# Performance work log

Hardware: AMD Instinct MI355X
Metric: run time of the kernel (lower is better)

## Reference

```python
import jax, jax.numpy as jnp
import numpy as np

B, L, S, D_MODEL, H = 2, 2048, 2048, 1024, 16
D_HEAD = D_MODEL // H  # 64


def setup_inputs() -> dict:
    key = jax.random.key(0)
    ks = jax.random.split(key, 11)
    s = 0.02
    return {
        "queries": jax.random.normal(ks[0], (B, L, D_MODEL), jnp.float32),
        "keys": jax.random.normal(ks[1], (B, S, D_MODEL), jnp.float32),
        "values": jax.random.normal(ks[2], (B, S, D_MODEL), jnp.float32),
        # Linear weights stored as [in, out] (torch W.T), biases [out]
        "Wq": jax.random.normal(ks[3], (D_MODEL, H * D_HEAD), jnp.float32) * s,
        "bq": jnp.zeros((H * D_HEAD,), jnp.float32),
        "Wk": jax.random.normal(ks[4], (D_MODEL, H * D_HEAD), jnp.float32) * s,
        "bk": jnp.zeros((H * D_HEAD,), jnp.float32),
        "Wv": jax.random.normal(ks[5], (D_MODEL, H * D_HEAD), jnp.float32) * s,
        "bv": jnp.zeros((H * D_HEAD,), jnp.float32),
        "Wo": jax.random.normal(ks[6], (H * D_HEAD, D_MODEL), jnp.float32) * s,
        "bo": jnp.zeros((D_MODEL,), jnp.float32),
    }


def reference(queries, keys, values, Wq, bq, Wk, bk, Wv, bv, Wo, bo):
    b, l, _ = queries.shape
    _, s, _ = keys.shape
    # QKV projections -> [B, L/S, H, D_HEAD]
    q = (queries @ Wq + bq).reshape(b, l, H, D_HEAD)
    k = (keys @ Wk + bk).reshape(b, s, H, D_HEAD)
    v = (values @ Wv + bv).reshape(b, s, H, D_HEAD)
    scale = 1.0 / jnp.sqrt(jnp.asarray(D_HEAD, q.dtype))
    # Full score matrix [B, H, L, S] (mask_flag=False -> no causal mask)
    scores = jnp.einsum("blhe,bshe->bhls", q, k)
    A = jax.nn.softmax(scale * scores, axis=-1)  # dropout is identity at eval
    out = jnp.einsum("bhls,bshd->blhd", A, v).reshape(b, l, H * D_HEAD)
    out = out @ Wo + bo
    return out, A
```

## Files before the change

### kernel.cpp

```cpp
#include <hip/hip_runtime.h>


typedef __attribute__((ext_vector_type(8))) __bf16 bf16x8;
typedef __attribute__((ext_vector_type(4))) float f32x4;

__device__ __forceinline__ unsigned int f2bf_u(float f) {
  unsigned int u = __float_as_uint(f);
  return (u + 0x7FFFu + ((u >> 16) & 1u)) >> 16;
}
__device__ __forceinline__ float bf2f(unsigned int h) {
  return __uint_as_float(h << 16);
}
__device__ __forceinline__ unsigned int pack2(float lo, float hi) {
  return (f2bf_u(hi) << 16) | f2bf_u(lo);
}
__device__ __forceinline__ f32x4 mfma16(bf16x8 a, bf16x8 b, f32x4 c) {
  return __builtin_amdgcn_mfma_f32_16x16x32_bf16(a, b, c, 0, 0, 0);
}
__device__ __forceinline__ void gll16(const void* g, void* l) {
  __builtin_amdgcn_global_load_lds(
      (const __attribute__((address_space(1))) unsigned int*)g,
      (__attribute__((address_space(3))) unsigned int*)l, 16, 0, 0);
}

__global__ __launch_bounds__(256) void transpose_w(
    const float* __restrict__ W0, const float* __restrict__ W1,
    const float* __restrict__ W2, const float* __restrict__ W3,
    unsigned short* __restrict__ T0, unsigned short* __restrict__ T1,
    unsigned short* __restrict__ T2, unsigned short* __restrict__ T3) {
  const float* W; unsigned short* T;
  switch (blockIdx.z) {
    case 0: W = W0; T = T0; break;
    case 1: W = W1; T = T1; break;
    case 2: W = W2; T = T2; break;
    default: W = W3; T = T3; break;
  }
  __shared__ float tile[32][33];
  const int tx = threadIdx.x, ty = threadIdx.y;
  const int i0 = blockIdx.x * 32, o0 = blockIdx.y * 32;
  #pragma unroll
  for (int r = 0; r < 4; ++r)
    tile[ty + 8 * r][tx] = W[(size_t)(i0 + ty + 8 * r) * 1024 + o0 + tx];
  __syncthreads();
  #pragma unroll
  for (int r = 0; r < 4; ++r)
    T[(size_t)(o0 + ty + 8 * r) * 1024 + i0 + tx] =
        (unsigned short)f2bf_u(tile[tx][ty + 8 * r]);
}

struct GemmJob {
  const float* A;
  const unsigned short* BT;
  const float* bias;
  void* C;
  int omode;
};
struct GemmJobs { GemmJob j[3]; };

__global__ __launch_bounds__(256) void gemm_qkv(GemmJobs jobs, int M, int N, int K) {
  const GemmJob jb = jobs.j[blockIdx.z];
  __shared__ unsigned short As[128][40];
  __shared__ unsigned short Bs[128][32];
  const int tid = threadIdx.x;
  const int lane = tid & 63, wid = tid >> 6;
  const int l15 = lane & 15, l4 = lane >> 4;
  const int m0 = blockIdx.x * 128, n0 = blockIdx.y * 128;
  const int wr = wid >> 1, wc = wid & 1;

  f32x4 acc[4][4];
  #pragma unroll
  for (int i = 0; i < 4; ++i)
    #pragma unroll
    for (int j = 0; j < 4; ++j) acc[i][j] = (f32x4){0.f, 0.f, 0.f, 0.f};

  const int nk = K >> 5;
  for (int kt = 0; kt < nk; ++kt) {
    #pragma unroll
    for (int c = 0; c < 4; ++c) {
      const int chunk = c * 256 + tid;
      const int row = chunk >> 3, col4 = chunk & 7;
      const float4 f = *(const float4*)(jb.A +
                                        (size_t)(m0 + row) * K + kt * 32 + col4 * 4);
      ushort4 o;
      o.x = (unsigned short)f2bf_u(f.x);
      o.y = (unsigned short)f2bf_u(f.y);
      o.z = (unsigned short)f2bf_u(f.z);
      o.w = (unsigned short)f2bf_u(f.w);
      *(ushort4*)&As[row][col4 * 4] = o;
    }
    #pragma unroll
    for (int c = 0; c < 2; ++c) {
      const int off = wid * 2048 + c * 1024;
      const int loff = off + lane * 16;
      const int row = loff >> 6, colb = loff & 63;
      gll16(jb.BT + (size_t)(n0 + row) * K + kt * 32 + colb / 2,
            (char*)&Bs[0][0] + off);
    }
    __syncthreads();
    bf16x8 af[4], bfr[4];
    #pragma unroll
    for (int i = 0; i < 4; ++i)
      af[i] = *(const bf16x8*)&As[wr * 64 + i * 16 + l15][l4 * 8];
    #pragma unroll
    for (int j = 0; j < 4; ++j)
      bfr[j] = *(const bf16x8*)&Bs[wc * 64 + j * 16 + l15][l4 * 8];
    #pragma unroll
    for (int i = 0; i < 4; ++i)
      #pragma unroll
      for (int j = 0; j < 4; ++j)
        acc[i][j] = mfma16(af[i], bfr[j], acc[i][j]);
    __syncthreads();
  }

  #pragma unroll
  for (int j = 0; j < 4; ++j) {
    const int col = n0 + wc * 64 + j * 16 + l15;
    const float bv = jb.bias[col];
    #pragma unroll
    for (int i = 0; i < 4; ++i) {
      const int rowb = m0 + wr * 64 + i * 16 + l4 * 4;
      if (jb.omode == 2) {
        const int bq = rowb >> 11, sq = rowb & 2047;
        const int hq = col >> 6, dq = col & 63;
        ushort4 o;
        o.x = (unsigned short)f2bf_u(acc[i][j][0] + bv);
        o.y = (unsigned short)f2bf_u(acc[i][j][1] + bv);
        o.z = (unsigned short)f2bf_u(acc[i][j][2] + bv);
        o.w = (unsigned short)f2bf_u(acc[i][j][3] + bv);
        *(ushort4*)((unsigned short*)jb.C +
                    ((size_t)((bq * 16 + hq) * 64 + dq) << 11) + sq) = o;
      } else {
        #pragma unroll
        for (int q = 0; q < 4; ++q)
          ((unsigned short*)jb.C)[(size_t)(rowb + q) * N + col] =
              (unsigned short)f2bf_u(acc[i][j][q] + bv);
      }
    }
  }
}

__global__ __launch_bounds__(256) void gemm_out(
    const unsigned short* __restrict__ Ap, const unsigned short* __restrict__ BT,
    const float* __restrict__ bias, float* __restrict__ Cp,
    int M, int N, int K) {
  __shared__ unsigned short As[128][32];
  __shared__ unsigned short Bs[128][32];
  const int tid = threadIdx.x;
  const int lane = tid & 63, wid = tid >> 6;
  const int l15 = lane & 15, l4 = lane >> 4;
  const int m0 = blockIdx.x * 128, n0 = blockIdx.y * 128;
  const int wr = wid >> 1, wc = wid & 1;

  f32x4 acc[4][4];
  #pragma unroll
  for (int i = 0; i < 4; ++i)
    #pragma unroll
    for (int j = 0; j < 4; ++j) acc[i][j] = (f32x4){0.f, 0.f, 0.f, 0.f};

  const int nk = K >> 5;
  for (int kt = 0; kt < nk; ++kt) {
    const unsigned short* G = (wid < 2) ? (Ap + (size_t)m0 * K)
                                        : (BT + (size_t)n0 * K);
    char* L = (wid < 2) ? (char*)&As[0][0] : (char*)&Bs[0][0];
    const int half = wid & 1;
    #pragma unroll
    for (int c = 0; c < 4; ++c) {
      const int off = half * 4096 + c * 1024;
      const int loff = off + lane * 16;
      const int row = loff >> 6, colb = loff & 63;
      gll16(G + (size_t)row * K + kt * 32 + colb / 2, L + off);
    }
    __syncthreads();
    bf16x8 af[4], bfr[4];
    #pragma unroll
    for (int i = 0; i < 4; ++i)
      af[i] = *(const bf16x8*)&As[wr * 64 + i * 16 + l15][l4 * 8];
    #pragma unroll
    for (int j = 0; j < 4; ++j)
      bfr[j] = *(const bf16x8*)&Bs[wc * 64 + j * 16 + l15][l4 * 8];
    #pragma unroll
    for (int i = 0; i < 4; ++i)
      #pragma unroll
      for (int j = 0; j < 4; ++j)
        acc[i][j] = mfma16(af[i], bfr[j], acc[i][j]);
    __syncthreads();
  }

  #pragma unroll
  for (int j = 0; j < 4; ++j) {
    const int col = n0 + wc * 64 + j * 16 + l15;
    const float bv = bias[col];
    #pragma unroll
    for (int i = 0; i < 4; ++i) {
      const int rowb = m0 + wr * 64 + i * 16 + l4 * 4;
      #pragma unroll
      for (int q = 0; q < 4; ++q)
        Cp[(size_t)(rowb + q) * N + col] = acc[i][j][q] + bv;
    }
  }
}

__global__ __launch_bounds__(512) void attn_pv(
    const unsigned short* __restrict__ Q, const unsigned short* __restrict__ K,
    const unsigned short* __restrict__ VT, float2* __restrict__ Mst,
    unsigned short* __restrict__ OutPre) {
  __shared__ unsigned short Kt[128][64];
  __shared__ unsigned short Vt[64][128];

  const int tid = threadIdx.x;
  const int w = tid >> 6, lane = tid & 63;
  const int l15 = lane & 15, l4 = lane >> 4;
  const int wgid = blockIdx.x;
  const int xcd = wgid & 7, j = wgid >> 3;
  const int bh = xcd * 4 + (j >> 4);
  const int b = bh >> 4, h = bh & 15;
  const int m0 = (j & 15) * 128;

  const unsigned short* Qp =
      Q + ((size_t)(b * 2048 + m0 + w * 16 + l15) << 10) + h * 64 + l4 * 8;
  const bf16x8 qf0 = *(const bf16x8*)Qp;
  const bf16x8 qf1 = *(const bf16x8*)(Qp + 32);

  const unsigned short* Kb = K + ((size_t)b << 21) + h * 64;
  const unsigned short* Vbh = VT + ((size_t)bh << 17);

  const int krow = lane >> 3;
  const int kcolb = (lane & 7) ^ krow;
  const int vrow = lane >> 4;

  float m_run = -3.0e38f, l_run = 0.f;
  f32x4 pv[4];
  #pragma unroll
  for (int nt = 0; nt < 4; ++nt) pv[nt] = (f32x4){0.f, 0.f, 0.f, 0.f};

  for (int t = 0; t < 16; ++t) {
    #pragma unroll
    for (int c = 0; c < 2; ++c) {
      const int r = w * 16 + c * 8 + krow;
      gll16(Kb + ((size_t)(t * 128 + r) << 10) + kcolb * 8,
            &Kt[w * 16 + c * 8][0]);
    }
    #pragma unroll
    for (int c = 0; c < 2; ++c) {
      const int d = w * 8 + c * 4 + vrow;
      const int vc = (lane & 15) ^ (d & 7);
      gll16(Vbh + ((size_t)d << 11) + t * 128 + vc * 8,
            &Vt[w * 8 + c * 4][0]);
    }
    __syncthreads();

    unsigned int sc16[16];
    float tmax = -3.0e38f;
    #pragma unroll
    for (int sub = 0; sub < 8; ++sub) {
      const int row = sub * 16 + l15;
      const bf16x8 k0 = *(const bf16x8*)&Kt[row][(l4 ^ (l15 & 7)) * 8];
      const bf16x8 k1 = *(const bf16x8*)&Kt[row][((l4 + 4) ^ (l15 & 7)) * 8];
      f32x4 a = {0.f, 0.f, 0.f, 0.f};
      a = mfma16(k0, qf0, a);
      a = mfma16(k1, qf1, a);
      const unsigned int u0 = f2bf_u(a[0] * 0.125f);
      const unsigned int u1 = f2bf_u(a[1] * 0.125f);
      const unsigned int u2 = f2bf_u(a[2] * 0.125f);
      const unsigned int u3 = f2bf_u(a[3] * 0.125f);
      sc16[sub * 2 + 0] = (u1 << 16) | u0;
      sc16[sub * 2 + 1] = (u3 << 16) | u2;
      tmax = fmaxf(tmax, fmaxf(fmaxf(bf2f(u0), bf2f(u1)),
                               fmaxf(bf2f(u2), bf2f(u3))));
    }
    tmax = fmaxf(tmax, __shfl_xor(tmax, 16));
    tmax = fmaxf(tmax, __shfl_xor(tmax, 32));
    const float m_new = fmaxf(m_run, tmax);
    const float f = __expf(m_run - m_new);
    m_run = m_new;
    float fr[4];
    #pragma unroll
    for (int r = 0; r < 4; ++r) fr[r] = __shfl(f, l4 * 4 + r);
    #pragma unroll
    for (int nt = 0; nt < 4; ++nt) {
      pv[nt][0] *= fr[0]; pv[nt][1] *= fr[1];
      pv[nt][2] *= fr[2]; pv[nt][3] *= fr[3];
    }
    l_run *= f;

    union EF { unsigned int u4[4]; bf16x8 v; } ef[4];
    #pragma unroll
    for (int kc = 0; kc < 4; ++kc) {
      #pragma unroll
      for (int half = 0; half < 2; ++half) {
        const unsigned int p0 = sc16[(kc * 2 + half) * 2 + 0];
        const unsigned int p1 = sc16[(kc * 2 + half) * 2 + 1];
        const float e0 = __expf(bf2f(p0 & 0xffffu) - m_new);
        const float e1 = __expf(bf2f(p0 >> 16) - m_new);
        const float e2 = __expf(bf2f(p1 & 0xffffu) - m_new);
        const float e3 = __expf(bf2f(p1 >> 16) - m_new);
        l_run += e0 + e1 + e2 + e3;
        ef[kc].u4[half * 2 + 0] = pack2(e0, e1);
        ef[kc].u4[half * 2 + 1] = pack2(e2, e3);
      }
    }

    #pragma unroll
    for (int nt = 0; nt < 4; ++nt) {
      const int d = nt * 16 + l15;
      #pragma unroll
      for (int kc = 0; kc < 4; ++kc) {
        const int c16a = (kc * 4 + (l4 >> 1)) ^ (d & 7);
        const int c16b = (kc * 4 + 2 + (l4 >> 1)) ^ (d & 7);
        union { unsigned int u4[4]; bf16x8 v; } vf;
        const uint2 va = *(const uint2*)&Vt[d][c16a * 8 + (l4 & 1) * 4];
        const uint2 vb = *(const uint2*)&Vt[d][c16b * 8 + (l4 & 1) * 4];
        vf.u4[0] = va.x; vf.u4[1] = va.y; vf.u4[2] = vb.x; vf.u4[3] = vb.y;
        pv[nt] = mfma16(ef[kc].v, vf.v, pv[nt]);
      }
    }
    __syncthreads();
  }

  float lsum = l_run;
  lsum += __shfl_xor(lsum, 16);
  lsum += __shfl_xor(lsum, 32);
  const float linv = 1.0f / lsum;
  if (lane < 16)
    Mst[(size_t)bh * 2048 + m0 + w * 16 + lane] = make_float2(m_run, linv);
  #pragma unroll
  for (int r = 0; r < 4; ++r) {
    const float lq = __shfl(linv, l4 * 4 + r);
    const size_t rowoff =
        ((size_t)(b * 2048 + m0 + w * 16 + l4 * 4 + r) << 10) + h * 64;
    #pragma unroll
    for (int nt = 0; nt < 4; ++nt)
      OutPre[rowoff + nt * 16 + l15] =
          (unsigned short)f2bf_u(pv[nt][r] * lq);
  }
}

__global__ __launch_bounds__(512) void attn_awrite(
    const unsigned short* __restrict__ Q, const unsigned short* __restrict__ K,
    const float2* __restrict__ Mst, float* __restrict__ Aout) {
  __shared__ float atile[16][136];
  const int tid = threadIdx.x;
  const int w = tid >> 6, lane = tid & 63;
  const int l15 = lane & 15, l4 = lane >> 4;
  const int wgid = blockIdx.x;
  const int xcd = wgid & 7, j = wgid >> 3;
  const int bh = xcd * 4 + (j >> 7);
  const int b = bh >> 4, h = bh & 15;
  const int m0 = (j & 127) * 16;

  const unsigned short* Qp =
      Q + ((size_t)(b * 2048 + m0 + l15) << 10) + h * 64 + l4 * 8;
  const bf16x8 qf0 = *(const bf16x8*)Qp;
  const bf16x8 qf1 = *(const bf16x8*)(Qp + 32);
  const unsigned short* Kb = K + ((size_t)b << 21) + h * 64;

  const float2 ml = Mst[(size_t)bh * 2048 + m0 + l15];
  const float mreg = ml.x, lreg = ml.y;

  float* Awg = Aout + ((size_t)bh << 22) + ((size_t)m0 << 11);
  const int frow = tid >> 5;
  const int fcol = (tid & 31) * 4;

  const unsigned short* kp0 = Kb + ((size_t)(w * 16 + l15) << 10) + l4 * 8;
  bf16x8 ck0 = *(const bf16x8*)kp0;
  bf16x8 ck1 = *(const bf16x8*)(kp0 + 32);
  #pragma unroll
  for (int i = 0; i < 16; ++i) {
    bf16x8 nk0, nk1;
    if (i < 15) {
      const unsigned short* kp =
          Kb + ((size_t)((i + 1) * 128 + w * 16 + l15) << 10) + l4 * 8;
      nk0 = *(const bf16x8*)kp;
      nk1 = *(const bf16x8*)(kp + 32);
    }
    f32x4 a = {0.f, 0.f, 0.f, 0.f};
    a = mfma16(ck0, qf0, a);
    a = mfma16(ck1, qf1, a);
    ck0 = nk0;
    ck1 = nk1;
    f32x4 av;
    #pragma unroll
    for (int q = 0; q < 4; ++q) {
      const float sb = bf2f(f2bf_u(a[q] * 0.125f));
      av[q] = __expf(sb - mreg) * lreg;
    }
    *(f32x4*)&atile[l15][w * 16 + l4 * 4] = av;
    __syncthreads();
    const f32x4 v = *(const f32x4*)&atile[frow][fcol];
    __builtin_nontemporal_store(
        v, (f32x4*)(Awg + ((size_t)frow << 11) + i * 128 + fcol));
    __syncthreads();
  }
}

extern "C" void kernel_launch(void* const* d_in, const int* in_sizes, int n_in,
                              void* d_out, int out_size, void* d_ws,
                              size_t ws_size, hipStream_t stream) {
  (void)in_sizes; (void)n_in; (void)out_size; (void)ws_size;
  const float* queries = (const float*)d_in[0];
  const float* keys    = (const float*)d_in[1];
  const float* values  = (const float*)d_in[2];
  const float* Wq = (const float*)d_in[3];  const float* bq = (const float*)d_in[4];
  const float* Wk = (const float*)d_in[5];  const float* bk = (const float*)d_in[6];
  const float* Wv = (const float*)d_in[7];  const float* bv = (const float*)d_in[8];
  const float* Wo = (const float*)d_in[9];  const float* bo = (const float*)d_in[10];

  float* out  = (float*)d_out;
  float* Aout = out + (size_t)2 * 2048 * 1024;

  char* ws = (char*)d_ws;
  unsigned short* WqT = (unsigned short*)(ws + 0);
  unsigned short* WkT = (unsigned short*)(ws + 2097152);
  unsigned short* WvT = (unsigned short*)(ws + 4194304);
  unsigned short* WoT = (unsigned short*)(ws + 6291456);
  unsigned short* Qb  = (unsigned short*)(ws + 8388608);
  unsigned short* Kbf = (unsigned short*)(ws + 16777216);
  unsigned short* VTb = (unsigned short*)(ws + 25165824);
  unsigned short* Op  = (unsigned short*)(ws + 33554432);
  float2* Mst = (float2*)(ws + 41943040);

  transpose_w<<<dim3(32, 32, 4), dim3(32, 8), 0, stream>>>(
      Wq, Wk, Wv, Wo, WqT, WkT, WvT, WoT);

  GemmJobs qkv;
  qkv.j[0] = {queries, WqT, bq, Qb, 0};
  qkv.j[1] = {keys,    WkT, bk, Kbf, 0};
  qkv.j[2] = {values,  WvT, bv, VTb, 2};
  gemm_qkv<<<dim3(32, 8, 3), 256, 0, stream>>>(qkv, 4096, 1024, 1024);

  attn_pv<<<dim3(512), 512, 0, stream>>>(Qb, Kbf, VTb, Mst, Op);
  attn_awrite<<<dim3(4096), 512, 0, stream>>>(Qb, Kbf, Mst, Aout);

  gemm_out<<<dim3(32, 8), 256, 0, stream>>>(
      Op, WoT, bo, out, 4096, 1024, 1024);
}
```

Baseline: 296.0 us.

## Double per-wave query rows in attn_pv and halve gemm_out N-tile

```diff
diff --git a/kernel.cpp b/kernel.cpp
--- a/kernel.cpp
+++ b/kernel.cpp
@@ -144,42 +144,45 @@
     const float* __restrict__ bias, float* __restrict__ Cp,
     int M, int N, int K) {
   __shared__ unsigned short As[128][32];
-  __shared__ unsigned short Bs[128][32];
+  __shared__ unsigned short Bs[64][32];
   const int tid = threadIdx.x;
-  const int lane = tid & 63, wid = tid >> 6;
+  const int lane = tid & 63, w = tid >> 6;
   const int l15 = lane & 15, l4 = lane >> 4;
-  const int m0 = blockIdx.x * 128, n0 = blockIdx.y * 128;
-  const int wr = wid >> 1, wc = wid & 1;
-
-  f32x4 acc[4][4];
-  #pragma unroll
-  for (int i = 0; i < 4; ++i)
+  const int m0 = blockIdx.x * 128, n0 = blockIdx.y * 64;
+
+  f32x4 acc[2][4];
+  #pragma unroll
+  for (int i = 0; i < 2; ++i)
     #pragma unroll
     for (int j = 0; j < 4; ++j) acc[i][j] = (f32x4){0.f, 0.f, 0.f, 0.f};
 
   const int nk = K >> 5;
   for (int kt = 0; kt < nk; ++kt) {
-    const unsigned short* G = (wid < 2) ? (Ap + (size_t)m0 * K)
-                                        : (BT + (size_t)n0 * K);
-    char* L = (wid < 2) ? (char*)&As[0][0] : (char*)&Bs[0][0];
-    const int half = wid & 1;
-    #pragma unroll
-    for (int c = 0; c < 4; ++c) {
-      const int off = half * 4096 + c * 1024;
+    #pragma unroll
+    for (int c = 0; c < 2; ++c) {
+      const int off = (w * 2 + c) * 1024;
       const int loff = off + lane * 16;
       const int row = loff >> 6, colb = loff & 63;
-      gll16(G + (size_t)row * K + kt * 32 + colb / 2, L + off);
-    }
-    __syncthreads();
-    bf16x8 af[4], bfr[4];
-    #pragma unroll
-    for (int i = 0; i < 4; ++i)
-      af[i] = *(const bf16x8*)&As[wr * 64 + i * 16 + l15][l4 * 8];
+      gll16(Ap + (size_t)(m0 + row) * K + kt * 32 + colb / 2,
+            (char*)&As[0][0] + off);
+    }
+    {
+      const int off = w * 1024;
+      const int loff = off + lane * 16;
+      const int row = loff >> 6, colb = loff & 63;
+      gll16(BT + (size_t)(n0 + row) * K + kt * 32 + colb / 2,
+            (char*)&Bs[0][0] + off);
+    }
+    __syncthreads();
+    bf16x8 af[2], bfr[4];
+    #pragma unroll
+    for (int i = 0; i < 2; ++i)
+      af[i] = *(const bf16x8*)&As[w * 32 + i * 16 + l15][l4 * 8];
     #pragma unroll
     for (int j = 0; j < 4; ++j)
-      bfr[j] = *(const bf16x8*)&Bs[wc * 64 + j * 16 + l15][l4 * 8];
-    #pragma unroll
-    for (int i = 0; i < 4; ++i)
+      bfr[j] = *(const bf16x8*)&Bs[j * 16 + l15][l4 * 8];
+    #pragma unroll
+    for (int i = 0; i < 2; ++i)
       #pragma unroll
       for (int j = 0; j < 4; ++j)
         acc[i][j] = mfma16(af[i], bfr[j], acc[i][j]);
@@ -188,11 +191,11 @@
 
   #pragma unroll
   for (int j = 0; j < 4; ++j) {
-    const int col = n0 + wc * 64 + j * 16 + l15;
+    const int col = n0 + j * 16 + l15;
     const float bv = bias[col];
     #pragma unroll
-    for (int i = 0; i < 4; ++i) {
-      const int rowb = m0 + wr * 64 + i * 16 + l4 * 4;
+    for (int i = 0; i < 2; ++i) {
+      const int rowb = m0 + w * 32 + i * 16 + l4 * 4;
       #pragma unroll
       for (int q = 0; q < 4; ++q)
         Cp[(size_t)(rowb + q) * N + col] = acc[i][j][q] + bv;
@@ -200,7 +203,7 @@
   }
 }
 
-__global__ __launch_bounds__(512) void attn_pv(
+__global__ __launch_bounds__(256) void attn_pv(
     const unsigned short* __restrict__ Q, const unsigned short* __restrict__ K,
     const unsigned short* __restrict__ VT, float2* __restrict__ Mst,
     unsigned short* __restrict__ OutPre) {
@@ -215,11 +218,16 @@
   const int bh = xcd * 4 + (j >> 4);
   const int b = bh >> 4, h = bh & 15;
   const int m0 = (j & 15) * 128;
-
-  const unsigned short* Qp =
-      Q + ((size_t)(b * 2048 + m0 + w * 16 + l15) << 10) + h * 64 + l4 * 8;
-  const bf16x8 qf0 = *(const bf16x8*)Qp;
-  const bf16x8 qf1 = *(const bf16x8*)(Qp + 32);
+  const int base = w * 32;
+
+  bf16x8 qf0[2], qf1[2];
+  #pragma unroll
+  for (int f = 0; f < 2; ++f) {
+    const unsigned short* Qp =
+        Q + ((size_t)(b * 2048 + m0 + base + f * 16 + l15) << 10) + h * 64 + l4 * 8;
+    qf0[f] = *(const bf16x8*)Qp;
+    qf1[f] = *(const bf16x8*)(Qp + 32);
+  }
 
   const unsigned short* Kb = K + ((size_t)b << 21) + h * 64;
   const unsigned short* Vbh = VT + ((size_t)bh << 17);
@@ -228,77 +236,88 @@
   const int kcolb = (lane & 7) ^ krow;
   const int vrow = lane >> 4;
 
-  float m_run = -3.0e38f, l_run = 0.f;
-  f32x4 pv[4];
-  #pragma unroll
-  for (int nt = 0; nt < 4; ++nt) pv[nt] = (f32x4){0.f, 0.f, 0.f, 0.f};
+  float m_run[2] = {-3.0e38f, -3.0e38f};
+  float l_run[2] = {0.f, 0.f};
+  f32x4 pv[2][4];
+  #pragma unroll
+  for (int f = 0; f < 2; ++f)
+    #pragma unroll
+    for (int nt = 0; nt < 4; ++nt) pv[f][nt] = (f32x4){0.f, 0.f, 0.f, 0.f};
 
   for (int t = 0; t < 16; ++t) {
     #pragma unroll
-    for (int c = 0; c < 2; ++c) {
-      const int r = w * 16 + c * 8 + krow;
+    for (int c = 0; c < 4; ++c) {
+      const int r = base + c * 8 + krow;
       gll16(Kb + ((size_t)(t * 128 + r) << 10) + kcolb * 8,
-            &Kt[w * 16 + c * 8][0]);
-    }
-    #pragma unroll
-    for (int c = 0; c < 2; ++c) {
-      const int d = w * 8 + c * 4 + vrow;
+            &Kt[base + c * 8][0]);
+    }
+    #pragma unroll
+    for (int c = 0; c < 4; ++c) {
+      const int d = w * 16 + c * 4 + vrow;
       const int vc = (lane & 15) ^ (d & 7);
       gll16(Vbh + ((size_t)d << 11) + t * 128 + vc * 8,
-            &Vt[w * 8 + c * 4][0]);
-    }
-    __syncthreads();
-
-    unsigned int sc16[16];
-    float tmax = -3.0e38f;
+            &Vt[w * 16 + c * 4][0]);
+    }
+    __syncthreads();
+
+    unsigned int sc16[2][16];
+    float tmax[2] = {-3.0e38f, -3.0e38f};
     #pragma unroll
     for (int sub = 0; sub < 8; ++sub) {
       const int row = sub * 16 + l15;
       const bf16x8 k0 = *(const bf16x8*)&Kt[row][(l4 ^ (l15 & 7)) * 8];
       const bf16x8 k1 = *(const bf16x8*)&Kt[row][((l4 + 4) ^ (l15 & 7)) * 8];
-      f32x4 a = {0.f, 0.f, 0.f, 0.f};
-      a = mfma16(k0, qf0, a);
-      a = mfma16(k1, qf1, a);
-      const unsigned int u0 = f2bf_u(a[0] * 0.125f);
-      const unsigned int u1 = f2bf_u(a[1] * 0.125f);
-      const unsigned int u2 = f2bf_u(a[2] * 0.125f);
-      const unsigned int u3 = f2bf_u(a[3] * 0.125f);
-      sc16[sub * 2 + 0] = (u1 << 16) | u0;
-      sc16[sub * 2 + 1] = (u3 << 16) | u2;
-      tmax = fmaxf(tmax, fmaxf(fmaxf(bf2f(u0), bf2f(u1)),
-                               fmaxf(bf2f(u2), bf2f(u3))));
-    }
-    tmax = fmaxf(tmax, __shfl_xor(tmax, 16));
-    tmax = fmaxf(tmax, __shfl_xor(tmax, 32));
-    const float m_new = fmaxf(m_run, tmax);
-    const float f = __expf(m_run - m_new);
-    m_run = m_new;
-    float fr[4];
-    #pragma unroll
-    for (int r = 0; r < 4; ++r) fr[r] = __shfl(f, l4 * 4 + r);
-    #pragma unroll
-    for (int nt = 0; nt < 4; ++nt) {
-      pv[nt][0] *= fr[0]; pv[nt][1] *= fr[1];
-      pv[nt][2] *= fr[2]; pv[nt][3] *= fr[3];
-    }
-    l_run *= f;
-
-    union EF { unsigned int u4[4]; bf16x8 v; } ef[4];
-    #pragma unroll
-    for (int kc = 0; kc < 4; ++kc) {
-      #pragma unroll
-      for (int half = 0; half < 2; ++half) {
-        const unsigned int p0 = sc16[(kc * 2 + half) * 2 + 0];
-        const unsigned int p1 = sc16[(kc * 2 + half) * 2 + 1];
-        const float e0 = __expf(bf2f(p0 & 0xffffu) - m_new);
-        const float e1 = __expf(bf2f(p0 >> 16) - m_new);
-        const float e2 = __expf(bf2f(p1 & 0xffffu) - m_new);
-        const float e3 = __expf(bf2f(p1 >> 16) - m_new);
-        l_run += e0 + e1 + e2 + e3;
-        ef[kc].u4[half * 2 + 0] = pack2(e0, e1);
-        ef[kc].u4[half * 2 + 1] = pack2(e2, e3);
+      #pragma unroll
+      for (int f = 0; f < 2; ++f) {
+        f32x4 a = {0.f, 0.f, 0.f, 0.f};
+        a = mfma16(k0, qf0[f], a);
+        a = mfma16(k1, qf1[f], a);
+        const unsigned int u0 = f2bf_u(a[0] * 0.125f);
+        const unsigned int u1 = f2bf_u(a[1] * 0.125f);
+        const unsigned int u2 = f2bf_u(a[2] * 0.125f);
+        const unsigned int u3 = f2bf_u(a[3] * 0.125f);
+        sc16[f][sub * 2 + 0] = (u1 << 16) | u0;
+        sc16[f][sub * 2 + 1] = (u3 << 16) | u2;
+        tmax[f] = fmaxf(tmax[f], fmaxf(fmaxf(bf2f(u0), bf2f(u1)),
+                                       fmaxf(bf2f(u2), bf2f(u3))));
       }
     }
+    #pragma unroll
+    for (int f = 0; f < 2; ++f) {
+      float tm = tmax[f];
+      tm = fmaxf(tm, __shfl_xor(tm, 16));
+      tm = fmaxf(tm, __shfl_xor(tm, 32));
+      const float m_new = fmaxf(m_run[f], tm);
+      const float fs = __expf(m_run[f] - m_new);
+      m_run[f] = m_new;
+      float fr[4];
+      #pragma unroll
+      for (int r = 0; r < 4; ++r) fr[r] = __shfl(fs, l4 * 4 + r);
+      #pragma unroll
+      for (int nt = 0; nt < 4; ++nt) {
+        pv[f][nt][0] *= fr[0]; pv[f][nt][1] *= fr[1];
+        pv[f][nt][2] *= fr[2]; pv[f][nt][3] *= fr[3];
+      }
+      l_run[f] *= fs;
+    }
+
+    union EF { unsigned int u4[4]; bf16x8 v; } ef[2][4];
+    #pragma unroll
+    for (int f = 0; f < 2; ++f)
+      #pragma unroll
+      for (int kc = 0; kc < 4; ++kc)
+        #pragma unroll
+        for (int half = 0; half < 2; ++half) {
+          const unsigned int p0 = sc16[f][(kc * 2 + half) * 2 + 0];
+          const unsigned int p1 = sc16[f][(kc * 2 + half) * 2 + 1];
+          const float e0 = __expf(bf2f(p0 & 0xffffu) - m_run[f]);
+          const float e1 = __expf(bf2f(p0 >> 16) - m_run[f]);
+          const float e2 = __expf(bf2f(p1 & 0xffffu) - m_run[f]);
+          const float e3 = __expf(bf2f(p1 >> 16) - m_run[f]);
+          l_run[f] += e0 + e1 + e2 + e3;
+          ef[f][kc].u4[half * 2 + 0] = pack2(e0, e1);
+          ef[f][kc].u4[half * 2 + 1] = pack2(e2, e3);
+        }
 
     #pragma unroll
     for (int nt = 0; nt < 4; ++nt) {
@@ -311,28 +330,38 @@
         const uint2 va = *(const uint2*)&Vt[d][c16a * 8 + (l4 & 1) * 4];
         const uint2 vb = *(const uint2*)&Vt[d][c16b * 8 + (l4 & 1) * 4];
         vf.u4[0] = va.x; vf.u4[1] = va.y; vf.u4[2] = vb.x; vf.u4[3] = vb.y;
-        pv[nt] = mfma16(ef[kc].v, vf.v, pv[nt]);
+        pv[0][nt] = mfma16(ef[0][kc].v, vf.v, pv[0][nt]);
+        pv[1][nt] = mfma16(ef[1][kc].v, vf.v, pv[1][nt]);
       }
     }
     __syncthreads();
   }
 
-  float lsum = l_run;
-  lsum += __shfl_xor(lsum, 16);
-  lsum += __shfl_xor(lsum, 32);
-  const float linv = 1.0f / lsum;
-  if (lane < 16)
-    Mst[(size_t)bh * 2048 + m0 + w * 16 + lane] = make_float2(m_run, linv);
-  #pragma unroll
-  for (int r = 0; r < 4; ++r) {
-    const float lq = __shfl(linv, l4 * 4 + r);
-    const size_t rowoff =
-        ((size_t)(b * 2048 + m0 + w * 16 + l4 * 4 + r) << 10) + h * 64;
-    #pragma unroll
-    for (int nt = 0; nt < 4; ++nt)
-      OutPre[rowoff + nt * 16 + l15] =
-          (unsigned short)f2bf_u(pv[nt][r] * lq);
-  }
+  float linv[2];
+  #pragma unroll
+  for (int f = 0; f < 2; ++f) {
+    float ls = l_run[f];
+    ls += __shfl_xor(ls, 16);
+    ls += __shfl_xor(ls, 32);
+    linv[f] = 1.0f / ls;
+  }
+  if (lane < 16) {
+    Mst[(size_t)bh * 2048 + m0 + base + lane] = make_float2(m_run[0], linv[0]);
+    Mst[(size_t)bh * 2048 + m0 + base + 16 + lane] =
+        make_float2(m_run[1], linv[1]);
+  }
+  #pragma unroll
+  for (int f = 0; f < 2; ++f)
+    #pragma unroll
+    for (int r = 0; r < 4; ++r) {
+      const float lq = __shfl(linv[f], l4 * 4 + r);
+      const size_t rowoff =
+          ((size_t)(b * 2048 + m0 + base + f * 16 + l4 * 4 + r) << 10) + h * 64;
+      #pragma unroll
+      for (int nt = 0; nt < 4; ++nt)
+        OutPre[rowoff + nt * 16 + l15] =
+            (unsigned short)f2bf_u(pv[f][nt][r] * lq);
+    }
 }
 
 __global__ __launch_bounds__(512) void attn_awrite(
@@ -428,9 +457,9 @@
   qkv.j[2] = {values,  WvT, bv, VTb, 2};
   gemm_qkv<<<dim3(32, 8, 3), 256, 0, stream>>>(qkv, 4096, 1024, 1024);
 
-  attn_pv<<<dim3(512), 512, 0, stream>>>(Qb, Kbf, VTb, Mst, Op);
+  attn_pv<<<dim3(512), 256, 0, stream>>>(Qb, Kbf, VTb, Mst, Op);
   attn_awrite<<<dim3(4096), 512, 0, stream>>>(Qb, Kbf, Mst, Aout);
 
-  gemm_out<<<dim3(32, 8), 256, 0, stream>>>(
+  gemm_out<<<dim3(32, 16), 256, 0, stream>>>(
       Op, WoT, bo, out, 4096, 1024, 1024);
 }
```

After: 294.5 us (median of 2 runs). No clear change (-0.5%).
